# Optimization experiments

Hardware: AMD Instinct MI355X
Metric: run time of the kernel (lower is better)

The kernel has to match this reference:

```python
import jax, jax.numpy as jnp
import numpy as np

B, T, D_IN, D_SAE, K = 1024, 4, 768, 8192, 32


def setup_inputs() -> dict:
    key = jax.random.key(0)
    k1, k2, k3 = jax.random.split(key, 3)
    x = jax.random.normal(k1, (B, T, D_IN), dtype=jnp.float32)
    W_enc = jax.random.normal(k2, (T, D_IN, D_SAE), dtype=jnp.float32) * (1.0 / D_IN ** 0.5)
    W_dec = jax.random.normal(k3, (D_SAE, T, D_IN), dtype=jnp.float32) * (1.0 / D_SAE ** 0.5)
    b_enc = jnp.zeros((D_SAE,), dtype=jnp.float32)
    b_dec = jnp.zeros((T, D_IN), dtype=jnp.float32)
    return {"x": x, "W_enc": W_enc, "W_dec": W_dec, "b_enc": b_enc, "b_dec": b_dec, "k": K}


def reference(x, W_enc, W_dec, b_enc, b_dec, k):
    # Encode: pre-activations over all dictionary atoms
    pre = jnp.einsum('btd,tds->bs', x, W_enc) + b_enc  # (B, d_sae)
    # TopK sparsity: keep top-k pre-activations per sample, relu them, zero the rest
    topk_vals, topk_idx = jax.lax.top_k(pre, k)        # (B, k)
    rows = jnp.arange(pre.shape[0])[:, None]           # (B, 1)
    z = jnp.zeros_like(pre).at[rows, topk_idx].set(jax.nn.relu(topk_vals))
    # Decode: dense einsum over all atoms (only k rows of W_dec actually contribute)
    x_hat = jnp.einsum('bs,std->btd', z, W_dec) + b_dec  # (B, T, d_in)
    # Reconstruction loss: sum over d_in, mean over (B, T)
    recon_loss = jnp.mean(jnp.sum((x_hat - x) ** 2, axis=-1))
    return recon_loss, x_hat, z
```

## Files before the change

### kernel.cpp

```cpp
#include <hip/hip_runtime.h>
#include <hip/hip_fp16.h>
#include <cfloat>

#define B_    1024
#define T_    4
#define DIN   768
#define KD    3072
#define DSAE  8192
#define TOPK  32

static constexpr size_t XHAT_OFF = 1;
static constexpr size_t Z_OFF    = 1 + (size_t)B_ * T_ * DIN;

typedef __attribute__((ext_vector_type(8))) short    frag;
typedef __attribute__((ext_vector_type(8))) _Float16 hfrag;
typedef __attribute__((ext_vector_type(4))) float    f32x4;

__device__ __forceinline__ unsigned pack2(float a, float b) {
    return (__builtin_bit_cast(unsigned, a) >> 16) | (__builtin_bit_cast(unsigned, b) & 0xFFFF0000u);
}
__device__ __forceinline__ float hi_part(float a) {
    return __builtin_bit_cast(float, __builtin_bit_cast(unsigned, a) & 0xFFFF0000u);
}

__global__ void zero_acc(double* acc) { if (threadIdx.x == 0) *acc = 0.0; }

__global__ __launch_bounds__(256) void convert_x(const float* __restrict__ x, ushort* __restrict__ Xh)
{
    const int row = blockIdx.y;
    const int col = blockIdx.x * 1024 + threadIdx.x * 4;
    const float4 f = *(const float4*)(x + (size_t)row * KD + col);
    ushort4 h;
    h.x = __half_as_ushort(__float2half(f.x));
    h.y = __half_as_ushort(__float2half(f.y));
    h.z = __half_as_ushort(__float2half(f.z));
    h.w = __half_as_ushort(__float2half(f.w));
    *(ushort4*)(Xh + (size_t)row * KD + col) = h;
}

__global__ __launch_bounds__(256) void convert_wT(const float* __restrict__ W, ushort* __restrict__ Wt)
{
    __shared__ float t[64][33];
    const int tx = threadIdx.x & 31, ty = threadIdx.x >> 5;
    const int n0 = blockIdx.x * 32, k0 = blockIdx.y * 64;
    #pragma unroll
    for (int j = 0; j < 8; j++)
        t[ty + j * 8][tx] = W[(size_t)(k0 + ty + j * 8) * DSAE + n0 + tx];
    __syncthreads();
    #pragma unroll
    for (int j = 0; j < 4; j++) {
        const int nl = ty + j * 8;
        const float a = t[tx * 2][nl], b = t[tx * 2 + 1][nl];
        const __half ha = __float2half(a), hb = __float2half(b);
        const float ra = (a - __half2float(ha)) * 2048.0f;
        const float rb = (b - __half2float(hb)) * 2048.0f;
        const ushort2 hv = make_ushort2(__half_as_ushort(ha), __half_as_ushort(hb));
        const ushort2 lv = make_ushort2(__half_as_ushort(__float2half(ra)),
                                        __half_as_ushort(__float2half(rb)));
        ushort* dst = Wt + (size_t)(n0 + nl) * (2 * KD) + k0 + tx * 2;
        *(ushort2*)dst        = hv;
        *(ushort2*)(dst + KD) = lv;
    }
}

__device__ __forceinline__ void gload16(const ushort* g, ushort* l)
{
    __builtin_amdgcn_global_load_lds((const __attribute__((address_space(1))) void*)g,
                                     (__attribute__((address_space(3))) void*)l, 16, 0, 0);
}

__global__ __launch_bounds__(256, 3) void encode_gemm(const ushort* __restrict__ Xh,
                                                      const ushort* __restrict__ Wt,
                                                      const float* __restrict__ benc,
                                                      float* __restrict__ pre)
{
    __shared__ ushort As [128 * 32];
    __shared__ ushort Bhs[128 * 32];

    const int tid  = threadIdx.x;
    const int n0   = blockIdx.x * 128, m0 = blockIdx.y * 128;
    const int lane = tid & 63, wv = tid >> 6;
    const int wrow = (wv >> 1) * 64, wcol = (wv & 1) * 64;
    const int lm = lane & 15, q = lane >> 4;

    f32x4 acc[4][4];
    #pragma unroll
    for (int i = 0; i < 4; i++)
        #pragma unroll
        for (int j = 0; j < 4; j++) acc[i][j] = (f32x4){0.f,0.f,0.f,0.f};

    const int srow = lane >> 2, scol = (lane & 3) * 8;
    const ushort* pa0 = Xh + (size_t)(m0 + wv * 16 + srow) * KD + scol;
    const ushort* pa1 = pa0 + (size_t)64 * KD;
    const ushort* pb0 = Wt + (size_t)(n0 + wv * 16 + srow) * (2 * KD) + scol;
    const ushort* pb1 = pb0 + (size_t)64 * (2 * KD);
    ushort* da0 = &As [wv * 512]; ushort* da1 = &As [2048 + wv * 512];
    ushort* dh0 = &Bhs[wv * 512]; ushort* dh1 = &Bhs[2048 + wv * 512];

    for (int k0 = 0; k0 < KD; k0 += 32) {
        gload16(pa0 + k0, da0);
        gload16(pa1 + k0, da1);
        gload16(pb0 + k0, dh0);
        gload16(pb1 + k0, dh1);
        __syncthreads();

        hfrag af[4], bh[4];
        #pragma unroll
        for (int t4 = 0; t4 < 4; t4++) {
            af[t4] = *(const hfrag*)&As [(wrow + t4 * 16 + lm) * 32 + q * 8];
            bh[t4] = *(const hfrag*)&Bhs[(wcol + t4 * 16 + lm) * 32 + q * 8];
        }
        #pragma unroll
        for (int mt = 0; mt < 4; mt++)
            #pragma unroll
            for (int nt = 0; nt < 4; nt++)
                acc[mt][nt] = __builtin_amdgcn_mfma_f32_16x16x32_f16(af[mt], bh[nt], acc[mt][nt], 0, 0, 0);
        __syncthreads();
    }

    #pragma unroll
    for (int mt = 0; mt < 4; mt++)
        #pragma unroll
        for (int nt = 0; nt < 4; nt++) {
            const int col = n0 + wcol + nt * 16 + lm;
            const float bv = benc[col];
            #pragma unroll
            for (int r = 0; r < 4; r++) {
                const int row = m0 + wrow + mt * 16 + q * 4 + r;
                pre[(size_t)row * DSAE + col] = acc[mt][nt][r] + bv;
            }
        }
}

#define PK 40
__global__ __launch_bounds__(256, 2) void encode_mfma(const float* __restrict__ x,
                                                      const float* __restrict__ W,
                                                      const float* __restrict__ benc,
                                                      float* __restrict__ pre)
{
    __shared__ short Ahi[128 * PK], Alo[128 * PK];
    __shared__ short Bhi[128 * PK], Blo[128 * PK];

    const int tid  = threadIdx.x;
    const int m0   = blockIdx.y * 128, n0 = blockIdx.x * 128;
    const int am = tid >> 1, ak = (tid & 1) << 4;
    const int bn = (tid & 31) << 2, bk = tid >> 5;
    const int lane = tid & 63, wv = tid >> 6;
    const int wrow = (wv >> 1) * 64, wcol = (wv & 1) * 64;
    const int lm = lane & 15, q = lane >> 4;

    f32x4 acc[4][4];
    #pragma unroll
    for (int i = 0; i < 4; i++)
        #pragma unroll
        for (int j = 0; j < 4; j++) acc[i][j] = (f32x4){0.f, 0.f, 0.f, 0.f};

    const float* pA0 = x + (size_t)(m0 + am) * KD + ak;
    const float* pB0 = W + (size_t)bk * 4 * DSAE + n0 + bn;

    for (int k0 = 0; k0 < KD; k0 += 32) {
        {
            const float* pA = pA0 + k0;
            float f[16];
            *(float4*)&f[0]  = *(const float4*)(pA);
            *(float4*)&f[4]  = *(const float4*)(pA + 4);
            *(float4*)&f[8]  = *(const float4*)(pA + 8);
            *(float4*)&f[12] = *(const float4*)(pA + 12);
            unsigned hw[8], lw[8];
            #pragma unroll
            for (int j = 0; j < 8; j++) {
                float a = f[2*j], b = f[2*j+1];
                float ha = hi_part(a), hb = hi_part(b);
                hw[j] = pack2(ha, hb);
                lw[j] = pack2(a - ha, b - hb);
            }
            short* dh = &Ahi[am * PK + ak];
            short* dl = &Alo[am * PK + ak];
            *(int4*)dh       = *(int4*)&hw[0];
            *(int4*)(dh + 8) = *(int4*)&hw[4];
            *(int4*)dl       = *(int4*)&lw[0];
            *(int4*)(dl + 8) = *(int4*)&lw[4];
        }
        {
            const float* pB = pB0 + (size_t)k0 * DSAE;
            float4 w0 = *(const float4*)(pB);
            float4 w1 = *(const float4*)(pB + DSAE);
            float4 w2 = *(const float4*)(pB + 2 * DSAE);
            float4 w3 = *(const float4*)(pB + 3 * DSAE);
            float fr[4][4] = {{w0.x,w0.y,w0.z,w0.w},{w1.x,w1.y,w1.z,w1.w},
                              {w2.x,w2.y,w2.z,w2.w},{w3.x,w3.y,w3.z,w3.w}};
            #pragma unroll
            for (int c = 0; c < 4; c++) {
                float h0 = hi_part(fr[0][c]), h1 = hi_part(fr[1][c]);
                float h2 = hi_part(fr[2][c]), h3 = hi_part(fr[3][c]);
                unsigned hh[2] = { pack2(h0, h1), pack2(h2, h3) };
                unsigned ll[2] = { pack2(fr[0][c]-h0, fr[1][c]-h1), pack2(fr[2][c]-h2, fr[3][c]-h3) };
                *(int2*)&Bhi[(bn + c) * PK + bk * 4] = *(int2*)&hh[0];
                *(int2*)&Blo[(bn + c) * PK + bk * 4] = *(int2*)&ll[0];
            }
        }
        __syncthreads();

        frag ah[4], al[4], bh[4], bl[4];
        #pragma unroll
        for (int t4 = 0; t4 < 4; t4++) {
            int r = (wrow + t4 * 16 + lm) * PK + q * 8;
            ah[t4] = *(const frag*)&Ahi[r];
            al[t4] = *(const frag*)&Alo[r];
            int cIdx = (wcol + t4 * 16 + lm) * PK + q * 8;
            bh[t4] = *(const frag*)&Bhi[cIdx];
            bl[t4] = *(const frag*)&Blo[cIdx];
        }
        #pragma unroll
        for (int mt = 0; mt < 4; mt++)
            #pragma unroll
            for (int nt = 0; nt < 4; nt++) {
                acc[mt][nt] = __builtin_amdgcn_mfma_f32_16x16x32_bf16(ah[mt], bh[nt], acc[mt][nt], 0, 0, 0);
                acc[mt][nt] = __builtin_amdgcn_mfma_f32_16x16x32_bf16(ah[mt], bl[nt], acc[mt][nt], 0, 0, 0);
                acc[mt][nt] = __builtin_amdgcn_mfma_f32_16x16x32_bf16(al[mt], bh[nt], acc[mt][nt], 0, 0, 0);
            }
        __syncthreads();
    }

    #pragma unroll
    for (int mt = 0; mt < 4; mt++)
        #pragma unroll
        for (int nt = 0; nt < 4; nt++) {
            int col = n0 + wcol + nt * 16 + lm;
            float bv = benc[col];
            #pragma unroll
            for (int r = 0; r < 4; r++) {
                int row = m0 + wrow + mt * 16 + q * 4 + r;
                pre[(size_t)row * DSAE + col] = acc[mt][nt][r] + bv;
            }
        }
}

__global__ __launch_bounds__(256) void select_topk(float* __restrict__ zout,
                                                   const float* __restrict__ x,
                                                   const float* __restrict__ W,
                                                   const ushort* __restrict__ Wt,
                                                   int* __restrict__ widx_g,
                                                   float* __restrict__ wval_g,
                                                   float mgn)
{
    const int b   = blockIdx.x;
    const int tid = threadIdx.x;

    __shared__ float vals[DSAE];
    __shared__ unsigned char flag[DSAE];
    __shared__ float lmax[256];
    __shared__ float cand_v[512]; __shared__ int cand_i[512];
    __shared__ float rv[256];  __shared__ int ri[256];
    __shared__ double dred[256];
    __shared__ float topv[TOPK]; __shared__ int topi[TOPK];
    __shared__ int wix[64]; __shared__ double wdv[64]; __shared__ unsigned char wsel[64];
    __shared__ int wcnt, nabove, outc, ncand;
    __shared__ float sL, sv32;

    float* zrow = zout + (size_t)b * DSAE;

    float lm = -FLT_MAX;
    #pragma unroll
    for (int p = 0; p < DSAE / 256; p++) {
        float v = zrow[tid + p * 256];
        vals[tid + p * 256] = v;
        lm = fmaxf(lm, v);
    }
    lmax[tid] = lm;
    if (tid == 0) { ncand = 0; wcnt = 0; nabove = 0; outc = 0; }
    __syncthreads();

    {
        int rk = 0;
        for (int j = 0; j < 256; j++) {
            float o = lmax[j];
            rk += (o > lm || (o == lm && j < tid)) ? 1 : 0;
        }
        if (rk == TOPK - 1) sL = lm;
    }
    __syncthreads();
    const float L = sL;

    for (int p = 0; p < DSAE / 256; p++) {
        int i = tid + p * 256;
        float v = vals[i];
        if (v > L) {
            int s = atomicAdd(&ncand, 1);
            if (s < 512) { cand_v[s] = v; cand_i[s] = i; }
        }
    }
    __syncthreads();
    const int ncg = ncand;

    if (ncg < TOPK) {
        if (tid == 0) sv32 = L;
    } else if (ncg <= 512) {
        for (int j = tid; j < ncg; j += 256) {
            float v = cand_v[j]; int idx = cand_i[j];
            int r = 0;
            for (int k2 = 0; k2 < ncg; k2++) {
                float o = cand_v[k2];
                r += (o > v || (o == v && cand_i[k2] < idx)) ? 1 : 0;
            }
            if (r == TOPK - 1) sv32 = v;
        }
    } else {
        for (int pass = 0; pass < TOPK; pass++) {
            float bv = -FLT_MAX; int bi = 0x7fffffff;
            for (int p = 0; p < DSAE / 256; p++) {
                int i = tid + p * 256;
                float v = vals[i];
                if (v > bv) { bv = v; bi = i; }
            }
            rv[tid] = bv; ri[tid] = bi; __syncthreads();
            for (int s = 128; s > 0; s >>= 1) {
                if (tid < s) {
                    if (rv[tid + s] > rv[tid] || (rv[tid + s] == rv[tid] && ri[tid + s] < ri[tid])) {
                        rv[tid] = rv[tid + s]; ri[tid] = ri[tid + s];
                    }
                }
                __syncthreads();
            }
            if (tid == 0) { topv[pass] = rv[0]; topi[pass] = ri[0]; vals[ri[0]] = -FLT_MAX; }
            __syncthreads();
        }
        if (tid < TOPK) vals[topi[tid]] = topv[tid];
        if (tid == 0) sv32 = topv[TOPK - 1];
    }
    __syncthreads();
    const float v32 = sv32;

    for (int p = 0; p < DSAE / 256; p++) {
        int i = tid + p * 256;
        float v = vals[i];
        if (v > v32 + mgn) { atomicAdd(&nabove, 1); }
        else if (v >= v32 - mgn) { int slot = atomicAdd(&wcnt, 1); if (slot < 64) wix[slot] = i; }
    }
    __syncthreads();
    const int nw   = wcnt < 64 ? wcnt : 64;
    const int need = TOPK - nabove;

    if (nw == need) {
        if (tid < 64) wsel[tid] = (tid < nw) ? 1 : 0;
    } else {
        const float* xr = x + (size_t)b * KD;
        for (int w = 0; w < nw; w++) {
            const int s = wix[w];
            double part = 0.0;
            if (Wt) {
                const ushort* wr = Wt + (size_t)s * (2 * KD);
                for (int kk = tid; kk < KD; kk += 256) {
                    double wvd = (double)__half2float(__ushort_as_half(wr[kk]))
                               + (double)__half2float(__ushort_as_half(wr[kk + KD])) * (1.0 / 2048.0);
                    part += (double)xr[kk] * wvd;
                }
            } else {
                for (int kk = tid; kk < KD; kk += 256)
                    part += (double)xr[kk] * (double)W[(size_t)kk * DSAE + s];
            }
            dred[tid] = part; __syncthreads();
            for (int st = 128; st > 0; st >>= 1) { if (tid < st) dred[tid] += dred[tid + st]; __syncthreads(); }
            if (tid == 0) wdv[w] = dred[0];
            __syncthreads();
        }
        if (tid < 64) {
            unsigned char sel = 0;
            if (tid < nw) {
                int rank = 0;
                double mv = wdv[tid]; int mi = wix[tid];
                for (int w2 = 0; w2 < nw; w2++)
                    if (wdv[w2] > mv || (wdv[w2] == mv && wix[w2] < mi)) rank++;
                sel = (rank < need) ? 1 : 0;
            }
            wsel[tid] = sel;
        }
    }
    __syncthreads();

    for (int p = 0; p < DSAE / 256; p++) flag[tid + p * 256] = 0;
    __syncthreads();
    for (int p = 0; p < DSAE / 256; p++) {
        int i = tid + p * 256;
        if (vals[i] > v32 + mgn) flag[i] = 1;
    }
    if (tid < nw && wsel[tid]) flag[wix[tid]] = 1;
    __syncthreads();

    for (int p = 0; p < DSAE / 256; p++) {
        int i = tid + p * 256;
        float v = vals[i];
        float zv = 0.f;
        if (flag[i]) {
            zv = v > 0.f ? v : 0.f;
            int slot = atomicAdd(&outc, 1);
            if (slot < TOPK) { widx_g[b * TOPK + slot] = i; wval_g[b * TOPK + slot] = zv; }
        }
        zrow[i] = zv;
    }
}

__global__ __launch_bounds__(256) void decode_loss(const int* __restrict__ widx_g,
                                                   const float* __restrict__ wval_g,
                                                   const float* __restrict__ Wdec,
                                                   const float* __restrict__ bdec,
                                                   const float* __restrict__ x,
                                                   float* __restrict__ xhat,
                                                   double* __restrict__ acc)
{
    const int b = blockIdx.x, tid = threadIdx.x;
    __shared__ int sidx[TOPK]; __shared__ float sval[TOPK];
    __shared__ double dred[256];
    if (tid < TOPK) { sidx[tid] = widx_g[b * TOPK + tid]; sval[tid] = wval_g[b * TOPK + tid]; }
    __syncthreads();

    float4 o[3];
    #pragma unroll
    for (int c = 0; c < 3; c++) o[c] = ((const float4*)bdec)[tid + c * 256];

    float4 wn[3];
    {
        const float4* wr = (const float4*)(Wdec + (size_t)sidx[0] * KD);
        #pragma unroll
        for (int c = 0; c < 3; c++) wn[c] = wr[tid + c * 256];
    }
    for (int j = 0; j < TOPK; j++) {
        const float v = sval[j];
        float4 w[3];
        #pragma unroll
        for (int c = 0; c < 3; c++) w[c] = wn[c];
        if (j + 1 < TOPK) {
            const float4* wr = (const float4*)(Wdec + (size_t)sidx[j + 1] * KD);
            #pragma unroll
            for (int c = 0; c < 3; c++) wn[c] = wr[tid + c * 256];
        }
        #pragma unroll
        for (int c = 0; c < 3; c++) {
            o[c].x = fmaf(v, w[c].x, o[c].x);
            o[c].y = fmaf(v, w[c].y, o[c].y);
            o[c].z = fmaf(v, w[c].z, o[c].z);
            o[c].w = fmaf(v, w[c].w, o[c].w);
        }
    }

    double ls = 0.0;
    const float4* xr = (const float4*)(x + (size_t)b * KD);
    float* xo = xhat + (size_t)b * KD;
    #pragma unroll
    for (int c = 0; c < 3; c++) {
        float4 xv = xr[tid + c * 256];
        float4 ov = o[c];
        float d0 = ov.x - xv.x, d1 = ov.y - xv.y, d2 = ov.z - xv.z, d3 = ov.w - xv.w;
        ls += (double)d0 * (double)d0 + (double)d1 * (double)d1
            + (double)d2 * (double)d2 + (double)d3 * (double)d3;
        const int e = (tid + c * 256) * 4;
        xo[e] = ov.x; xo[e + 1] = ov.y; xo[e + 2] = ov.z; xo[e + 3] = ov.w;
    }
    dred[tid] = ls; __syncthreads();
    for (int s = 128; s > 0; s >>= 1) { if (tid < s) dred[tid] += dred[tid + s]; __syncthreads(); }
    if (tid == 0) atomicAdd(acc, dred[0]);
}

__global__ void finalize(const double* __restrict__ acc, float* __restrict__ out)
{
    if (threadIdx.x == 0) out[0] = (float)(*acc / (double)(B_ * T_));
}

extern "C" void kernel_launch(void* const* d_in, const int* in_sizes, int n_in,
                              void* d_out, int out_size, void* d_ws, size_t ws_size,
                              hipStream_t stream)
{
    (void)in_sizes; (void)n_in; (void)out_size;
    const float* x    = (const float*)d_in[0];
    const float* Wenc = (const float*)d_in[1];
    const float* Wdec = (const float*)d_in[2];
    const float* benc = (const float*)d_in[3];
    const float* bdec = (const float*)d_in[4];

    float*  out    = (float*)d_out;
    double* acc    = (double*)d_ws;
    int*    widx_g = (int*)((char*)d_ws + 16);
    float*  wval_g = (float*)((char*)d_ws + 16 + (size_t)B_ * TOPK * 4);

    const size_t XC_OFF = (size_t)1 << 20;
    const size_t WT_OFF = (size_t)8 << 20;
    const size_t NEED   = WT_OFF + (size_t)DSAE * (2 * KD) * 2;
    const bool fast = (ws_size >= NEED);

    float* pre  = out + Z_OFF;
    float* xhat = out + XHAT_OFF;

    hipLaunchKernelGGL(zero_acc, dim3(1), dim3(1), 0, stream, acc);

    ushort* Xh = (ushort*)((char*)d_ws + XC_OFF);
    ushort* Wt = (ushort*)((char*)d_ws + WT_OFF);
    if (fast) {
        hipLaunchKernelGGL(convert_x,   dim3(3, B_),            dim3(256), 0, stream, x, Xh);
        hipLaunchKernelGGL(convert_wT,  dim3(DSAE/32, KD/64),   dim3(256), 0, stream, Wenc, Wt);
        hipLaunchKernelGGL(encode_gemm, dim3(DSAE/128, B_/128), dim3(256), 0, stream, Xh, Wt, benc, pre);
    } else {
        hipLaunchKernelGGL(encode_mfma, dim3(DSAE/128, B_/128), dim3(256), 0, stream, x, Wenc, benc, pre);
    }

    hipLaunchKernelGGL(select_topk, dim3(B_), dim3(256), 0, stream, pre, x, Wenc,
                       fast ? Wt : (const ushort*)nullptr, widx_g, wval_g,
                       fast ? 1.25e-2f : 2e-3f);
    hipLaunchKernelGGL(decode_loss, dim3(B_), dim3(256), 0, stream, widx_g, wval_g, Wdec, bdec, x, xhat, acc);
    hipLaunchKernelGGL(finalize,    dim3(1),  dim3(1),   0, stream, acc, out);
}
```

Measured before the change: 426.4 us.

## Add register-resident top-k select kernel with separate pre buffer, fold zero_acc

Adds a new top-k selection kernel that keeps each row's pre-activations in registers. It finds a threshold from per-thread maxima, gathers candidates above it and ranks them, and writes z directly. Pre-activations go to a separate workspace buffer, so the output z region is written only once. The acc zeroing is folded into convert_x to drop one launch, and decode_loss now uses 384 threads per block. A new workspace tier is required, and the path falls back to the old kernels when the workspace is too small.

Result: no change. 420.5 us (-1.4%).

```diff
diff --git a/kernel.cpp b/kernel.cpp
--- a/kernel.cpp
+++ b/kernel.cpp
@@ -25,8 +25,10 @@
 
 __global__ void zero_acc(double* acc) { if (threadIdx.x == 0) *acc = 0.0; }
 
-__global__ __launch_bounds__(256) void convert_x(const float* __restrict__ x, ushort* __restrict__ Xh)
-{
+__global__ __launch_bounds__(256) void convert_x(const float* __restrict__ x, ushort* __restrict__ Xh,
+                                                 double* __restrict__ acc)
+{
+    if (blockIdx.x == 0 && blockIdx.y == 0 && threadIdx.x == 0) *acc = 0.0;
     const int row = blockIdx.y;
     const int col = blockIdx.x * 1024 + threadIdx.x * 4;
     const float4 f = *(const float4*)(x + (size_t)row * KD + col);
@@ -234,6 +236,176 @@
                 pre[(size_t)row * DSAE + col] = acc[mt][nt][r] + bv;
             }
         }
+}
+
+__global__ __launch_bounds__(256) void select_topk_fast(const float* __restrict__ pre,
+                                                        float* __restrict__ zout,
+                                                        const float* __restrict__ x,
+                                                        const ushort* __restrict__ Wt,
+                                                        int* __restrict__ widx_g,
+                                                        float* __restrict__ wval_g,
+                                                        float mgn)
+{
+    const int b = blockIdx.x, tid = threadIdx.x;
+
+    __shared__ float lmax[256];
+    __shared__ float cand_v[512]; __shared__ int cand_i[512];
+    __shared__ float rv[256]; __shared__ int ri[256];
+    __shared__ int wix[64]; __shared__ double wdv[64]; __shared__ unsigned char wsel[64];
+    __shared__ int selix[64];
+    __shared__ int wcnt, nabove, outc, ncand, nsel;
+    __shared__ float sL, sv32;
+
+    const float4* pre4 = (const float4*)(pre + (size_t)b * DSAE);
+    float4 r[8];
+    float lm = -FLT_MAX;
+    #pragma unroll
+    for (int p = 0; p < 8; p++) {
+        r[p] = pre4[p * 256 + tid];
+        lm = fmaxf(fmaxf(fmaxf(lm, r[p].x), fmaxf(r[p].y, r[p].z)), r[p].w);
+    }
+    lmax[tid] = lm;
+    if (tid == 0) { ncand = 0; wcnt = 0; nabove = 0; outc = 0; nsel = 0; }
+    __syncthreads();
+
+    {
+        int rk = 0;
+        for (int j = 0; j < 256; j++) {
+            float o = lmax[j];
+            rk += (o > lm || (o == lm && j < tid)) ? 1 : 0;
+        }
+        if (rk == TOPK - 1) sL = lm;
+    }
+    __syncthreads();
+    const float L = sL;
+
+    #pragma unroll
+    for (int p = 0; p < 8; p++) {
+        const int base = (p * 256 + tid) * 4;
+        const float vv[4] = {r[p].x, r[p].y, r[p].z, r[p].w};
+        #pragma unroll
+        for (int c = 0; c < 4; c++)
+            if (vv[c] > L) {
+                int s = atomicAdd(&ncand, 1);
+                if (s < 512) { cand_v[s] = vv[c]; cand_i[s] = base + c; }
+            }
+    }
+    __syncthreads();
+    const int ncg = ncand;
+
+    if (ncg < TOPK) {
+        if (tid == 0) sv32 = L;
+    } else if (ncg <= 512) {
+        for (int j = tid; j < ncg; j += 256) {
+            float v = cand_v[j]; int idx = cand_i[j];
+            int rr = 0;
+            for (int k2 = 0; k2 < ncg; k2++) {
+                float o = cand_v[k2];
+                rr += (o > v || (o == v && cand_i[k2] < idx)) ? 1 : 0;
+            }
+            if (rr == TOPK - 1) sv32 = v;
+        }
+    } else {
+        unsigned tmask = 0;
+        for (int pass = 0; pass < TOPK; pass++) {
+            float bv = -FLT_MAX; int bi = 0x7fffffff;
+            #pragma unroll
+            for (int p = 0; p < 8; p++) {
+                const int base = (p * 256 + tid) * 4;
+                const float vv[4] = {r[p].x, r[p].y, r[p].z, r[p].w};
+                #pragma unroll
+                for (int c = 0; c < 4; c++)
+                    if (!((tmask >> (p * 4 + c)) & 1u) && vv[c] > bv) { bv = vv[c]; bi = base + c; }
+            }
+            rv[tid] = bv; ri[tid] = bi; __syncthreads();
+            for (int s = 128; s > 0; s >>= 1) {
+                if (tid < s) {
+                    if (rv[tid + s] > rv[tid] || (rv[tid + s] == rv[tid] && ri[tid + s] < ri[tid])) {
+                        rv[tid] = rv[tid + s]; ri[tid] = ri[tid + s];
+                    }
+                }
+                __syncthreads();
+            }
+            const int gi = ri[0];
+            if (tid == ((gi >> 2) & 255)) tmask |= 1u << (((gi >> 10) << 2) | (gi & 3));
+            if (tid == 0 && pass == TOPK - 1) sv32 = rv[0];
+            __syncthreads();
+        }
+    }
+    __syncthreads();
+    const float v32 = sv32;
+
+    #pragma unroll
+    for (int p = 0; p < 8; p++) {
+        const int base = (p * 256 + tid) * 4;
+        const float vv[4] = {r[p].x, r[p].y, r[p].z, r[p].w};
+        #pragma unroll
+        for (int c = 0; c < 4; c++) {
+            const float v = vv[c];
+            if (v > v32 + mgn) { atomicAdd(&nabove, 1); }
+            else if (v >= v32 - mgn) { int slot = atomicAdd(&wcnt, 1); if (slot < 64) wix[slot] = base + c; }
+        }
+    }
+    __syncthreads();
+    const int nw   = wcnt < 64 ? wcnt : 64;
+    const int need = TOPK - nabove;
+
+    if (nw == need) {
+        if (tid < 64) wsel[tid] = (tid < nw) ? 1 : 0;
+    } else {
+        const float* xr = x + (size_t)b * KD;
+        const int wvId = tid >> 6, lane = tid & 63;
+        for (int w = wvId; w < nw; w += 4) {
+            const ushort* wr = Wt + (size_t)wix[w] * (2 * KD);
+            double part = 0.0;
+            for (int kk = lane; kk < KD; kk += 64) {
+                double wvd = (double)__half2float(__ushort_as_half(wr[kk]))
+                           + (double)__half2float(__ushort_as_half(wr[kk + KD])) * (1.0 / 2048.0);
+                part += (double)xr[kk] * wvd;
+            }
+            #pragma unroll
+            for (int off = 32; off > 0; off >>= 1) part += __shfl_down(part, off);
+            if (lane == 0) wdv[w] = part;
+        }
+        __syncthreads();
+        if (tid < 64) {
+            unsigned char sel = 0;
+            if (tid < nw) {
+                int rank = 0;
+                double mv = wdv[tid]; int mi = wix[tid];
+                for (int w2 = 0; w2 < nw; w2++)
+                    if (wdv[w2] > mv || (wdv[w2] == mv && wix[w2] < mi)) rank++;
+                sel = (rank < need) ? 1 : 0;
+            }
+            wsel[tid] = sel;
+        }
+    }
+    __syncthreads();
+
+    if (tid < nw && wsel[tid]) { int s = atomicAdd(&nsel, 1); selix[s] = wix[tid]; }
+    __syncthreads();
+    const int ns = nsel;
+
+    float* zrow = zout + (size_t)b * DSAE;
+    #pragma unroll
+    for (int p = 0; p < 8; p++) {
+        const int base = (p * 256 + tid) * 4;
+        const float vv[4] = {r[p].x, r[p].y, r[p].z, r[p].w};
+        #pragma unroll
+        for (int c = 0; c < 4; c++) {
+            const float v = vv[c];
+            bool pick = (v > v32 + mgn);
+            if (!pick && v >= v32 - mgn)
+                for (int s2 = 0; s2 < ns; s2++) pick = pick || (selix[s2] == base + c);
+            float zv = 0.f;
+            if (pick) {
+                zv = v > 0.f ? v : 0.f;
+                int slot = atomicAdd(&outc, 1);
+                if (slot < TOPK) { widx_g[b * TOPK + slot] = base + c; wval_g[b * TOPK + slot] = zv; }
+            }
+            zrow[base + c] = zv;
+        }
+    }
 }
 
 __global__ __launch_bounds__(256) void select_topk(float* __restrict__ zout,
@@ -400,7 +572,7 @@
     }
 }
 
-__global__ __launch_bounds__(256) void decode_loss(const int* __restrict__ widx_g,
+__global__ __launch_bounds__(384) void decode_loss(const int* __restrict__ widx_g,
                                                    const float* __restrict__ wval_g,
                                                    const float* __restrict__ Wdec,
                                                    const float* __restrict__ bdec,
@@ -410,32 +582,32 @@
 {
     const int b = blockIdx.x, tid = threadIdx.x;
     __shared__ int sidx[TOPK]; __shared__ float sval[TOPK];
-    __shared__ double dred[256];
+    __shared__ double dred[384];
     if (tid < TOPK) { sidx[tid] = widx_g[b * TOPK + tid]; sval[tid] = wval_g[b * TOPK + tid]; }
     __syncthreads();
 
-    float4 o[3];
-    #pragma unroll
-    for (int c = 0; c < 3; c++) o[c] = ((const float4*)bdec)[tid + c * 256];
-
-    float4 wn[3];
+    float4 o[2];
+    #pragma unroll
+    for (int c = 0; c < 2; c++) o[c] = ((const float4*)bdec)[tid + c * 384];
+
+    float4 wn[2];
     {
         const float4* wr = (const float4*)(Wdec + (size_t)sidx[0] * KD);
         #pragma unroll
-        for (int c = 0; c < 3; c++) wn[c] = wr[tid + c * 256];
+        for (int c = 0; c < 2; c++) wn[c] = wr[tid + c * 384];
     }
     for (int j = 0; j < TOPK; j++) {
         const float v = sval[j];
-        float4 w[3];
-        #pragma unroll
-        for (int c = 0; c < 3; c++) w[c] = wn[c];
+        float4 w[2];
+        #pragma unroll
+        for (int c = 0; c < 2; c++) w[c] = wn[c];
         if (j + 1 < TOPK) {
             const float4* wr = (const float4*)(Wdec + (size_t)sidx[j + 1] * KD);
             #pragma unroll
-            for (int c = 0; c < 3; c++) wn[c] = wr[tid + c * 256];
-        }
-        #pragma unroll
-        for (int c = 0; c < 3; c++) {
+            for (int c = 0; c < 2; c++) wn[c] = wr[tid + c * 384];
+        }
+        #pragma unroll
+        for (int c = 0; c < 2; c++) {
             o[c].x = fmaf(v, w[c].x, o[c].x);
             o[c].y = fmaf(v, w[c].y, o[c].y);
             o[c].z = fmaf(v, w[c].z, o[c].z);
@@ -447,16 +619,18 @@
     const float4* xr = (const float4*)(x + (size_t)b * KD);
     float* xo = xhat + (size_t)b * KD;
     #pragma unroll
-    for (int c = 0; c < 3; c++) {
-        float4 xv = xr[tid + c * 256];
+    for (int c = 0; c < 2; c++) {
+        float4 xv = xr[tid + c * 384];
         float4 ov = o[c];
         float d0 = ov.x - xv.x, d1 = ov.y - xv.y, d2 = ov.z - xv.z, d3 = ov.w - xv.w;
         ls += (double)d0 * (double)d0 + (double)d1 * (double)d1
             + (double)d2 * (double)d2 + (double)d3 * (double)d3;
-        const int e = (tid + c * 256) * 4;
+        const int e = (tid + c * 384) * 4;
         xo[e] = ov.x; xo[e + 1] = ov.y; xo[e + 2] = ov.z; xo[e + 3] = ov.w;
     }
     dred[tid] = ls; __syncthreads();
+    if (tid < 128) dred[tid] += dred[tid + 256];
+    __syncthreads();
     for (int s = 128; s > 0; s >>= 1) { if (tid < s) dred[tid] += dred[tid + s]; __syncthreads(); }
     if (tid == 0) atomicAdd(acc, dred[0]);
 }
@@ -482,29 +656,38 @@
     int*    widx_g = (int*)((char*)d_ws + 16);
     float*  wval_g = (float*)((char*)d_ws + 16 + (size_t)B_ * TOPK * 4);
 
-    const size_t XC_OFF = (size_t)1 << 20;
-    const size_t WT_OFF = (size_t)8 << 20;
-    const size_t NEED   = WT_OFF + (size_t)DSAE * (2 * KD) * 2;
-    const bool fast = (ws_size >= NEED);
-
-    float* pre  = out + Z_OFF;
+    const size_t XC_OFF    = (size_t)1 << 20;
+    const size_t PRE_OFF   = (size_t)8 << 20;
+    const size_t WT_OFF_F  = PRE_OFF + (size_t)B_ * DSAE * 4;
+    const size_t NEED_FULL = WT_OFF_F + (size_t)DSAE * (2 * KD) * 2;
+    const size_t WT_OFF_M  = (size_t)8 << 20;
+    const size_t NEED_MID  = WT_OFF_M + (size_t)DSAE * (2 * KD) * 2;
+    const int tier = (ws_size >= NEED_FULL) ? 2 : (ws_size >= NEED_MID ? 1 : 0);
+
+    float* zreg = out + Z_OFF;
     float* xhat = out + XHAT_OFF;
 
-    hipLaunchKernelGGL(zero_acc, dim3(1), dim3(1), 0, stream, acc);
-
-    ushort* Xh = (ushort*)((char*)d_ws + XC_OFF);
-    ushort* Wt = (ushort*)((char*)d_ws + WT_OFF);
-    if (fast) {
-        hipLaunchKernelGGL(convert_x,   dim3(3, B_),            dim3(256), 0, stream, x, Xh);
+    if (tier >= 1) {
+        ushort* Xh = (ushort*)((char*)d_ws + XC_OFF);
+        ushort* Wt = (ushort*)((char*)d_ws + (tier == 2 ? WT_OFF_F : WT_OFF_M));
+        float*  pre = (tier == 2) ? (float*)((char*)d_ws + PRE_OFF) : zreg;
+
+        hipLaunchKernelGGL(convert_x,   dim3(3, B_),            dim3(256), 0, stream, x, Xh, acc);
         hipLaunchKernelGGL(convert_wT,  dim3(DSAE/32, KD/64),   dim3(256), 0, stream, Wenc, Wt);
         hipLaunchKernelGGL(encode_gemm, dim3(DSAE/128, B_/128), dim3(256), 0, stream, Xh, Wt, benc, pre);
+        if (tier == 2)
+            hipLaunchKernelGGL(select_topk_fast, dim3(B_), dim3(256), 0, stream,
+                               pre, zreg, x, Wt, widx_g, wval_g, 1.25e-2f);
+        else
+            hipLaunchKernelGGL(select_topk, dim3(B_), dim3(256), 0, stream,
+                               zreg, x, Wenc, Wt, widx_g, wval_g, 1.25e-2f);
     } else {
-        hipLaunchKernelGGL(encode_mfma, dim3(DSAE/128, B_/128), dim3(256), 0, stream, x, Wenc, benc, pre);
-    }
-
-    hipLaunchKernelGGL(select_topk, dim3(B_), dim3(256), 0, stream, pre, x, Wenc,
-                       fast ? Wt : (const ushort*)nullptr, widx_g, wval_g,
-                       fast ? 1.25e-2f : 2e-3f);
-    hipLaunchKernelGGL(decode_loss, dim3(B_), dim3(256), 0, stream, widx_g, wval_g, Wdec, bdec, x, xhat, acc);
+        hipLaunchKernelGGL(zero_acc,    dim3(1),                dim3(1),   0, stream, acc);
+        hipLaunchKernelGGL(encode_mfma, dim3(DSAE/128, B_/128), dim3(256), 0, stream, x, Wenc, benc, zreg);
+        hipLaunchKernelGGL(select_topk, dim3(B_), dim3(256), 0, stream,
+                           zreg, x, Wenc, (const ushort*)nullptr, widx_g, wval_g, 2e-3f);
+    }
+
+    hipLaunchKernelGGL(decode_loss, dim3(B_), dim3(384), 0, stream, widx_g, wval_g, Wdec, bdec, x, xhat, acc);
     hipLaunchKernelGGL(finalize,    dim3(1),  dim3(1),   0, stream, acc, out);
 }
```
